# Kernel optimization log

Hardware: AMD Instinct MI355X
Metric: run time of the kernel (lower is better)

## Reference

```python
import jax, jax.numpy as jnp
import numpy as np

HIDDEN = 2048
N_HEADS = 16
N_KV_HEADS = 4
HEAD_DIM = HIDDEN // N_HEADS  # 128
BATCH = 2
SEQ = 2048


def setup_inputs() -> dict:
    key = jax.random.key(0)
    ks = jax.random.split(key, 10)
    s = 0.02
    return {
        "hidden_states": jax.random.normal(ks[0], (BATCH, SEQ, HIDDEN), jnp.float32),
        "attention_mask": jnp.ones((BATCH, SEQ), jnp.int32),
        # weights stored [in, out] so y = x @ W + b (transpose of torch layout)
        "Wq": jax.random.normal(ks[1], (HIDDEN, N_HEADS * HEAD_DIM), jnp.float32) * s,
        "bq": jnp.zeros((N_HEADS * HEAD_DIM,), jnp.float32),
        "Wk": jax.random.normal(ks[2], (HIDDEN, N_KV_HEADS * HEAD_DIM), jnp.float32) * s,
        "bk": jnp.zeros((N_KV_HEADS * HEAD_DIM,), jnp.float32),
        "Wv": jax.random.normal(ks[3], (HIDDEN, N_KV_HEADS * HEAD_DIM), jnp.float32) * s,
        "bv": jnp.zeros((N_KV_HEADS * HEAD_DIM,), jnp.float32),
        "Wo": jax.random.normal(ks[4], (N_HEADS * HEAD_DIM, HIDDEN), jnp.float32) * s,
        "bo": jnp.zeros((HIDDEN,), jnp.float32),
    }


def reference(hidden_states, attention_mask, Wq, bq, Wk, bk, Wv, bv, Wo, bo):
    B, S, _ = hidden_states.shape
    q = hidden_states @ Wq + bq  # [B,S,H*D]
    k = hidden_states @ Wk + bk  # [B,S,Hkv*D]
    v = hidden_states @ Wv + bv

    q = q.reshape(B, S, N_HEADS, HEAD_DIM).transpose(0, 2, 1, 3)      # [B,H,S,D]
    k = k.reshape(B, S, N_KV_HEADS, HEAD_DIM).transpose(0, 2, 1, 3)   # [B,Hkv,S,D]
    v = v.reshape(B, S, N_KV_HEADS, HEAD_DIM).transpose(0, 2, 1, 3)

    # GQA: repeat_interleave along head dim (head h uses kv head h // groups)
    groups = N_HEADS // N_KV_HEADS
    k = jnp.repeat(k, groups, axis=1)  # [B,H,S,D]
    v = jnp.repeat(v, groups, axis=1)

    scale = 1.0 / np.sqrt(HEAD_DIM)
    scores = jnp.einsum('bhqd,bhkd->bhqk', q, k) * scale  # [B,H,S,S]

    causal = jnp.tril(jnp.ones((S, S), bool))              # True = keep
    keep = causal[None, None, :, :] & (attention_mask[:, None, None, :] != 0)
    scores = jnp.where(keep, scores, -jnp.inf)

    attn = jax.nn.softmax(scores.astype(jnp.float32), axis=-1).astype(q.dtype)
    out = jnp.einsum('bhqk,bhkd->bhqd', attn, v)            # [B,H,S,D]
    out = out.transpose(0, 2, 1, 3).reshape(B, S, N_HEADS * HEAD_DIM)
    return out @ Wo + bo
```

## Files before the change

kernel.cpp:

```cpp
#include <hip/hip_runtime.h>
#include <hip/hip_bf16.h>


typedef unsigned short u16;
typedef __attribute__((ext_vector_type(8))) short short8;
typedef __attribute__((ext_vector_type(4))) float f32x4;

#define BATCH 2
#define SEQ 2048
#define HIDDEN 2048
#define NH 16
#define NKV 4
#define HD 128
#define QKV_N 3072
#define MROWS 4096

__device__ inline u16 f2bf(float f) {
    __hip_bfloat16 h = __float2bfloat16(f);
    return __builtin_bit_cast(u16, h);
}

__device__ inline void async_copy16(const u16* g, u16* lds_base) {
    __builtin_amdgcn_global_load_lds(
        (const __attribute__((address_space(1))) void*)g,
        (__attribute__((address_space(3))) void*)lds_base, 16, 0, 0);
}

__global__ void convert_f32_bf16(const float* __restrict__ src, u16* __restrict__ dst, int n) {
    int i = (blockIdx.x * 256 + threadIdx.x) * 4;
    if (i + 3 < n) {
        float4 v = *(const float4*)(src + i);
        dst[i + 0] = f2bf(v.x);
        dst[i + 1] = f2bf(v.y);
        dst[i + 2] = f2bf(v.z);
        dst[i + 3] = f2bf(v.w);
    }
}

__global__ void transpose_f32_bf16(const float* __restrict__ src, u16* __restrict__ dst,
                                   int K, int N) {
    __shared__ float tile[32][33];
    int n0 = blockIdx.x * 32, k0 = blockIdx.y * 32;
    int tx = threadIdx.x, ty = threadIdx.y;
#pragma unroll
    for (int i = 0; i < 32; i += 8)
        tile[ty + i][tx] = src[(size_t)(k0 + ty + i) * N + n0 + tx];
    __syncthreads();
#pragma unroll
    for (int i = 0; i < 32; i += 8)
        dst[(size_t)(n0 + ty + i) * K + k0 + tx] = f2bf(tile[tx][ty + i]);
}

__global__ void build_bias(const float* __restrict__ bq, const float* __restrict__ bk,
                           const float* __restrict__ bv, float* __restrict__ bqkv) {
    int i = blockIdx.x * 256 + threadIdx.x;
    if (i < QKV_N)
        bqkv[i] = (i < 2048) ? bq[i] : ((i < 2560) ? bk[i - 2048] : bv[i - 2560]);
}

__global__ void vt_from_qkv(const u16* __restrict__ qkv, u16* __restrict__ vt) {
    __shared__ u16 tile[32][33];
    int b = blockIdx.z >> 2, kvh = blockIdx.z & 3;
    int s0 = blockIdx.x * 32, d0 = blockIdx.y * 32;
    int tx = threadIdx.x, ty = threadIdx.y;
#pragma unroll
    for (int i = 0; i < 32; i += 8)
        tile[ty + i][tx] = qkv[(size_t)(b * SEQ + s0 + ty + i) * QKV_N + 2560 + kvh * HD + d0 + tx];
    __syncthreads();
#pragma unroll
    for (int i = 0; i < 32; i += 8)
        vt[(size_t)((b * NKV + kvh) * HD + d0 + ty + i) * SEQ + s0 + tx] = tile[tx][ty + i];
}

template <bool OUT_BF16>
__global__ __launch_bounds__(256)
void gemm_bf16_128(const u16* __restrict__ A, const u16* __restrict__ BT,
                   const float* __restrict__ bias, void* __restrict__ outp,
                   int M, int N, int K) {
    __shared__ __align__(16) u16 As[128][32];
    __shared__ __align__(16) u16 Bs[128][32];
    int t = threadIdx.x, w = t >> 6, lane = t & 63, quad = lane >> 4, l16 = lane & 15;
    int wm = w & 1, wn = w >> 1;
    int bm0 = blockIdx.y * 128, bn0 = blockIdx.x * 128;

    f32x4 acc[4][4];
#pragma unroll
    for (int i = 0; i < 4; i++)
#pragma unroll
        for (int j = 0; j < 4; j++) acc[i][j] = (f32x4){0.f, 0.f, 0.f, 0.f};

    for (int k0 = 0; k0 < K; k0 += 32) {
        __syncthreads();
#pragma unroll
        for (int j = 0; j < 2; j++) {
            int f = (w * 2 + j) * 64 + lane;
            int row = f >> 2, col = (f & 3) * 8;
            u16* abase = &As[0][0] + (size_t)(w * 2 + j) * 512;
            u16* bbase = &Bs[0][0] + (size_t)(w * 2 + j) * 512;
            async_copy16(A + (size_t)(bm0 + row) * K + k0 + col, abase);
            async_copy16(BT + (size_t)(bn0 + row) * K + k0 + col, bbase);
        }
        __syncthreads();
        short8 af[4], bf[4];
#pragma unroll
        for (int mt = 0; mt < 4; mt++) af[mt] = *(const short8*)(&As[wm * 64 + mt * 16 + l16][quad * 8]);
#pragma unroll
        for (int nt = 0; nt < 4; nt++) bf[nt] = *(const short8*)(&Bs[wn * 64 + nt * 16 + l16][quad * 8]);
#pragma unroll
        for (int mt = 0; mt < 4; mt++)
#pragma unroll
            for (int nt = 0; nt < 4; nt++)
                acc[mt][nt] = __builtin_amdgcn_mfma_f32_16x16x32_bf16(af[mt], bf[nt], acc[mt][nt], 0, 0, 0);
    }
#pragma unroll
    for (int nt = 0; nt < 4; nt++) {
        int col = bn0 + wn * 64 + nt * 16 + l16;
        float bcol = bias[col];
#pragma unroll
        for (int mt = 0; mt < 4; mt++) {
#pragma unroll
            for (int r = 0; r < 4; r++) {
                int row = bm0 + wm * 64 + mt * 16 + quad * 4 + r;
                float v = acc[mt][nt][r] + bcol;
                if constexpr (OUT_BF16)
                    ((u16*)outp)[(size_t)row * N + col] = f2bf(v);
                else
                    ((float*)outp)[(size_t)row * N + col] = v;
            }
        }
    }
}

__global__ __launch_bounds__(512, 4)
void flash_attn(const u16* __restrict__ qkv, const u16* __restrict__ vt,
                const int* __restrict__ amask, u16* __restrict__ attn) {
    __shared__ __align__(16) u16 Ks[64][136];
    __shared__ __align__(16) u16 Vs[128][72];
    __shared__ __align__(16) u16 Pb[8][16][72];
    int t = threadIdx.x, w = t >> 6, lane = t & 63, quad = lane >> 4, l16 = lane & 15;
    int bx = blockIdx.x, b = blockIdx.z;
    int qt = b ? ((int)gridDim.x - 1 - bx) : bx;
    int h = blockIdx.y, kvh = h >> 2;
    int q_row0 = qt * 128 + w * 16;
    u16(*P)[72] = Pb[w];

    const u16* qrow = qkv + (size_t)(b * SEQ + q_row0 + l16) * QKV_N + h * HD;
    short8 qf[4];
#pragma unroll
    for (int c = 0; c < 4; c++) qf[c] = *(const short8*)(qrow + c * 32 + quad * 8);

    f32x4 o[8];
#pragma unroll
    for (int dt = 0; dt < 8; dt++) o[dt] = (f32x4){0.f, 0.f, 0.f, 0.f};
    float lpart[4] = {0.f, 0.f, 0.f, 0.f};

    const float scale2 = 0.12751743f;
    const float C2 = 14.4269504f;

    const u16* kgb = qkv + (size_t)(b * SEQ) * QKV_N + 2048 + kvh * HD;
    const u16* vgb = vt + (size_t)((b * NKV + kvh) * HD) * SEQ;
    const int* am = amask + b * SEQ;

    int kr = t >> 4, kc = (t & 15) * 8;
    int vr = t >> 3, vc = (t & 7) * 8;
    int kb_end = (qt + 1) * 128;

    short8 k0p, k1p, v0p, v1p;
    {
        const u16* kg = kgb;
        const u16* vg = vgb;
        k0p = *(const short8*)(kg + (size_t)kr * QKV_N + kc);
        k1p = *(const short8*)(kg + (size_t)(kr + 32) * QKV_N + kc);
        v0p = *(const short8*)(vg + (size_t)vr * SEQ + vc);
        v1p = *(const short8*)(vg + (size_t)(vr + 64) * SEQ + vc);
    }

    for (int kb = 0; kb < kb_end; kb += 64) {
        __syncthreads();
        *(short8*)(&Ks[kr][kc]) = k0p;
        *(short8*)(&Ks[kr + 32][kc]) = k1p;
        *(short8*)(&Vs[vr][vc]) = v0p;
        *(short8*)(&Vs[vr + 64][vc]) = v1p;
        __syncthreads();
        if (kb + 64 < kb_end) {
            const u16* kg = kgb + (size_t)(kb + 64) * QKV_N;
            const u16* vg = vgb + kb + 64;
            k0p = *(const short8*)(kg + (size_t)kr * QKV_N + kc);
            k1p = *(const short8*)(kg + (size_t)(kr + 32) * QKV_N + kc);
            v0p = *(const short8*)(vg + (size_t)vr * SEQ + vc);
            v1p = *(const short8*)(vg + (size_t)(vr + 64) * SEQ + vc);
        }
        if (kb > q_row0 + 15) continue;

        f32x4 sc[4];
#pragma unroll
        for (int nt = 0; nt < 4; nt++) sc[nt] = (f32x4){0.f, 0.f, 0.f, 0.f};
#pragma unroll
        for (int c = 0; c < 4; c++) {
#pragma unroll
            for (int nt = 0; nt < 4; nt++) {
                short8 kf = *(const short8*)(&Ks[nt * 16 + l16][c * 32 + quad * 8]);
                sc[nt] = __builtin_amdgcn_mfma_f32_16x16x32_bf16(qf[c], kf, sc[nt], 0, 0, 0);
            }
        }

        int kidx = kb + l16;
        int mk0 = am[kidx], mk1 = am[kidx + 16], mk2 = am[kidx + 32], mk3 = am[kidx + 48];
#pragma unroll
        for (int r = 0; r < 4; r++) {
            int qi = q_row0 + quad * 4 + r;
            float v0 = (mk0 && kidx      <= qi) ? sc[0][r] : -INFINITY;
            float v1 = (mk1 && kidx + 16 <= qi) ? sc[1][r] : -INFINITY;
            float v2 = (mk2 && kidx + 32 <= qi) ? sc[2][r] : -INFINITY;
            float v3 = (mk3 && kidx + 48 <= qi) ? sc[3][r] : -INFINITY;
            float p0 = __builtin_exp2f(__builtin_fmaf(v0, scale2, -C2));
            float p1 = __builtin_exp2f(__builtin_fmaf(v1, scale2, -C2));
            float p2 = __builtin_exp2f(__builtin_fmaf(v2, scale2, -C2));
            float p3 = __builtin_exp2f(__builtin_fmaf(v3, scale2, -C2));
            lpart[r] += (p0 + p1) + (p2 + p3);
            P[quad * 4 + r][l16]      = f2bf(p0);
            P[quad * 4 + r][16 + l16] = f2bf(p1);
            P[quad * 4 + r][32 + l16] = f2bf(p2);
            P[quad * 4 + r][48 + l16] = f2bf(p3);
        }
        asm volatile("s_waitcnt lgkmcnt(0)" ::: "memory");
        short8 pf0 = *(const short8*)(&P[l16][quad * 8]);
        short8 pf1 = *(const short8*)(&P[l16][32 + quad * 8]);
#pragma unroll
        for (int dt = 0; dt < 8; dt++) {
            short8 vf0 = *(const short8*)(&Vs[dt * 16 + l16][quad * 8]);
            o[dt] = __builtin_amdgcn_mfma_f32_16x16x32_bf16(pf0, vf0, o[dt], 0, 0, 0);
            short8 vf1 = *(const short8*)(&Vs[dt * 16 + l16][32 + quad * 8]);
            o[dt] = __builtin_amdgcn_mfma_f32_16x16x32_bf16(pf1, vf1, o[dt], 0, 0, 0);
        }
    }
    float inv[4];
#pragma unroll
    for (int r = 0; r < 4; r++) {
        float l = lpart[r];
#pragma unroll
        for (int off = 1; off < 16; off <<= 1) l += __shfl_xor(l, off, 64);
        inv[r] = l > 0.f ? 1.f / l : 0.f;
    }
    size_t obase = (size_t)(b * SEQ + q_row0) * HIDDEN + h * HD;
#pragma unroll
    for (int dt = 0; dt < 8; dt++)
#pragma unroll
        for (int r = 0; r < 4; r++)
            attn[obase + (size_t)(quad * 4 + r) * HIDDEN + dt * 16 + l16] = f2bf(o[dt][r] * inv[r]);
}

extern "C" void kernel_launch(void* const* d_in, const int* in_sizes, int n_in,
                              void* d_out, int out_size, void* d_ws, size_t ws_size,
                              hipStream_t stream) {
    const float* hidden = (const float*)d_in[0];
    const int* amask   = (const int*)d_in[1];
    const float* Wq = (const float*)d_in[2];
    const float* bq = (const float*)d_in[3];
    const float* Wk = (const float*)d_in[4];
    const float* bk = (const float*)d_in[5];
    const float* Wv = (const float*)d_in[6];
    const float* bv = (const float*)d_in[7];
    const float* Wo = (const float*)d_in[8];
    const float* bo = (const float*)d_in[9];
    float* out = (float*)d_out;

    char* ws = (char*)d_ws;
    u16* xb     = (u16*)ws;  ws += (size_t)MROWS * HIDDEN * 2;
    u16* wqkvT  = (u16*)ws;  ws += (size_t)QKV_N * HIDDEN * 2;
    u16* woT    = (u16*)ws;  ws += (size_t)HIDDEN * HIDDEN * 2;
    float* bqkv = (float*)ws; ws += (size_t)QKV_N * 4;
    u16* qkv    = (u16*)ws;  ws += (size_t)MROWS * QKV_N * 2;
    u16* vt     = (u16*)ws;  ws += (size_t)BATCH * NKV * HD * SEQ * 2;
    u16* attn   = (u16*)ws;  ws += (size_t)MROWS * HIDDEN * 2;

    convert_f32_bf16<<<dim3(MROWS * HIDDEN / 1024), dim3(256), 0, stream>>>(hidden, xb, MROWS * HIDDEN);
    transpose_f32_bf16<<<dim3(64, 64), dim3(32, 8), 0, stream>>>(Wq, wqkvT, HIDDEN, 2048);
    transpose_f32_bf16<<<dim3(16, 64), dim3(32, 8), 0, stream>>>(Wk, wqkvT + (size_t)2048 * HIDDEN, HIDDEN, 512);
    transpose_f32_bf16<<<dim3(16, 64), dim3(32, 8), 0, stream>>>(Wv, wqkvT + (size_t)2560 * HIDDEN, HIDDEN, 512);
    transpose_f32_bf16<<<dim3(64, 64), dim3(32, 8), 0, stream>>>(Wo, woT, HIDDEN, HIDDEN);
    build_bias<<<dim3(12), dim3(256), 0, stream>>>(bq, bk, bv, bqkv);

    gemm_bf16_128<true><<<dim3(QKV_N / 128, MROWS / 128), dim3(256), 0, stream>>>(
        xb, wqkvT, bqkv, qkv, MROWS, QKV_N, HIDDEN);

    vt_from_qkv<<<dim3(SEQ / 32, HD / 32, BATCH * NKV), dim3(32, 8), 0, stream>>>(qkv, vt);

    flash_attn<<<dim3(SEQ / 128, NH, BATCH), dim3(512), 0, stream>>>(qkv, vt, amask, attn);

    gemm_bf16_128<false><<<dim3(HIDDEN / 128, MROWS / 128), dim3(256), 0, stream>>>(
        attn, woT, bo, out, MROWS, HIDDEN, HIDDEN);
}
```

Before: 346.0 us.

## Permute K tile rows so P writes pack four adjacent keys per lane

K rows are loaded into LDS in a permuted order, so each lane's four score columns map to four consecutive keys. This lets the mask be read as one int4 and each P row be written as a single packed 8-byte store instead of four scattered 2-byte stores. The first-half V fragments are now prefetched before the LDS wait, the MFMA sections are wrapped in s_setprio, and the f32-to-bf16 conversion kernel uses vector stores. The permutation has to agree exactly with how the P·V MFMA reads its operands, otherwise the output is wrong. Holding the prefetched V fragments also raises register pressure.

Measured after the change: 338.3 us. -2.2%, faster.

```diff
diff --git a/kernel.cpp b/kernel.cpp
--- a/kernel.cpp
+++ b/kernel.cpp
@@ -30,10 +30,9 @@
     int i = (blockIdx.x * 256 + threadIdx.x) * 4;
     if (i + 3 < n) {
         float4 v = *(const float4*)(src + i);
-        dst[i + 0] = f2bf(v.x);
-        dst[i + 1] = f2bf(v.y);
-        dst[i + 2] = f2bf(v.z);
-        dst[i + 3] = f2bf(v.w);
+        ushort4 o;
+        o.x = f2bf(v.x); o.y = f2bf(v.y); o.z = f2bf(v.z); o.w = f2bf(v.w);
+        *(ushort4*)(dst + i) = o;
     }
 }
 
@@ -162,17 +161,16 @@
     const int* am = amask + b * SEQ;
 
     int kr = t >> 4, kc = (t & 15) * 8;
+    int ksrc = 4 * (kr & 15) + (kr >> 4);
     int vr = t >> 3, vc = (t & 7) * 8;
     int kb_end = (qt + 1) * 128;
 
     short8 k0p, k1p, v0p, v1p;
     {
-        const u16* kg = kgb;
-        const u16* vg = vgb;
-        k0p = *(const short8*)(kg + (size_t)kr * QKV_N + kc);
-        k1p = *(const short8*)(kg + (size_t)(kr + 32) * QKV_N + kc);
-        v0p = *(const short8*)(vg + (size_t)vr * SEQ + vc);
-        v1p = *(const short8*)(vg + (size_t)(vr + 64) * SEQ + vc);
+        k0p = *(const short8*)(kgb + (size_t)ksrc * QKV_N + kc);
+        k1p = *(const short8*)(kgb + (size_t)(ksrc + 2) * QKV_N + kc);
+        v0p = *(const short8*)(vgb + (size_t)vr * SEQ + vc);
+        v1p = *(const short8*)(vgb + (size_t)(vr + 64) * SEQ + vc);
     }
 
     for (int kb = 0; kb < kb_end; kb += 64) {
@@ -185,8 +183,8 @@
         if (kb + 64 < kb_end) {
             const u16* kg = kgb + (size_t)(kb + 64) * QKV_N;
             const u16* vg = vgb + kb + 64;
-            k0p = *(const short8*)(kg + (size_t)kr * QKV_N + kc);
-            k1p = *(const short8*)(kg + (size_t)(kr + 32) * QKV_N + kc);
+            k0p = *(const short8*)(kg + (size_t)ksrc * QKV_N + kc);
+            k1p = *(const short8*)(kg + (size_t)(ksrc + 2) * QKV_N + kc);
             v0p = *(const short8*)(vg + (size_t)vr * SEQ + vc);
             v1p = *(const short8*)(vg + (size_t)(vr + 64) * SEQ + vc);
         }
@@ -195,6 +193,7 @@
         f32x4 sc[4];
 #pragma unroll
         for (int nt = 0; nt < 4; nt++) sc[nt] = (f32x4){0.f, 0.f, 0.f, 0.f};
+        __builtin_amdgcn_s_setprio(1);
 #pragma unroll
         for (int c = 0; c < 4; c++) {
 #pragma unroll
@@ -203,36 +202,44 @@
                 sc[nt] = __builtin_amdgcn_mfma_f32_16x16x32_bf16(qf[c], kf, sc[nt], 0, 0, 0);
             }
         }
-
-        int kidx = kb + l16;
-        int mk0 = am[kidx], mk1 = am[kidx + 16], mk2 = am[kidx + 32], mk3 = am[kidx + 48];
+        __builtin_amdgcn_s_setprio(0);
+
+        int kbase = kb + 4 * l16;
+        int4 mk = *(const int4*)(am + kbase);
 #pragma unroll
         for (int r = 0; r < 4; r++) {
             int qi = q_row0 + quad * 4 + r;
-            float v0 = (mk0 && kidx      <= qi) ? sc[0][r] : -INFINITY;
-            float v1 = (mk1 && kidx + 16 <= qi) ? sc[1][r] : -INFINITY;
-            float v2 = (mk2 && kidx + 32 <= qi) ? sc[2][r] : -INFINITY;
-            float v3 = (mk3 && kidx + 48 <= qi) ? sc[3][r] : -INFINITY;
+            float v0 = (mk.x && kbase     <= qi) ? sc[0][r] : -INFINITY;
+            float v1 = (mk.y && kbase + 1 <= qi) ? sc[1][r] : -INFINITY;
+            float v2 = (mk.z && kbase + 2 <= qi) ? sc[2][r] : -INFINITY;
+            float v3 = (mk.w && kbase + 3 <= qi) ? sc[3][r] : -INFINITY;
             float p0 = __builtin_exp2f(__builtin_fmaf(v0, scale2, -C2));
             float p1 = __builtin_exp2f(__builtin_fmaf(v1, scale2, -C2));
             float p2 = __builtin_exp2f(__builtin_fmaf(v2, scale2, -C2));
             float p3 = __builtin_exp2f(__builtin_fmaf(v3, scale2, -C2));
             lpart[r] += (p0 + p1) + (p2 + p3);
-            P[quad * 4 + r][l16]      = f2bf(p0);
-            P[quad * 4 + r][16 + l16] = f2bf(p1);
-            P[quad * 4 + r][32 + l16] = f2bf(p2);
-            P[quad * 4 + r][48 + l16] = f2bf(p3);
-        }
+            uint2 pk;
+            pk.x = (unsigned)f2bf(p0) | ((unsigned)f2bf(p1) << 16);
+            pk.y = (unsigned)f2bf(p2) | ((unsigned)f2bf(p3) << 16);
+            *(uint2*)(&P[quad * 4 + r][4 * l16]) = pk;
+        }
+        short8 vf0[8];
+#pragma unroll
+        for (int dt = 0; dt < 8; dt++)
+            vf0[dt] = *(const short8*)(&Vs[dt * 16 + l16][quad * 8]);
         asm volatile("s_waitcnt lgkmcnt(0)" ::: "memory");
         short8 pf0 = *(const short8*)(&P[l16][quad * 8]);
         short8 pf1 = *(const short8*)(&P[l16][32 + quad * 8]);
+        __builtin_amdgcn_s_setprio(1);
+#pragma unroll
+        for (int dt = 0; dt < 8; dt++)
+            o[dt] = __builtin_amdgcn_mfma_f32_16x16x32_bf16(pf0, vf0[dt], o[dt], 0, 0, 0);
 #pragma unroll
         for (int dt = 0; dt < 8; dt++) {
-            short8 vf0 = *(const short8*)(&Vs[dt * 16 + l16][quad * 8]);
-            o[dt] = __builtin_amdgcn_mfma_f32_16x16x32_bf16(pf0, vf0, o[dt], 0, 0, 0);
             short8 vf1 = *(const short8*)(&Vs[dt * 16 + l16][32 + quad * 8]);
             o[dt] = __builtin_amdgcn_mfma_f32_16x16x32_bf16(pf1, vf1, o[dt], 0, 0, 0);
         }
+        __builtin_amdgcn_s_setprio(0);
     }
     float inv[4];
 #pragma unroll
```
